# Performance work log

Hardware: AMD Instinct MI355X
Metric: run time of the kernel (lower is better)

The kernel has to match this reference:

```python
import jax, jax.numpy as jnp
import numpy as np

EMBED_DIM = 1024
NUM_HEADS = 16
HEAD_DIM = EMBED_DIM // NUM_HEADS  # 64
KV_RANK = 64
QK_RANK = 64
EPS = 1e-6


def rmsnorm(x, w):
    var = jnp.mean(x * x, axis=-1, keepdims=True)
    return x * jax.lax.rsqrt(var + EPS) * w


def setup_inputs() -> dict:
    key = jax.random.key(0)
    ks = jax.random.split(key, 6)
    B, N, C = 4, 2048, EMBED_DIM
    s = lambda fan_in: 1.0 / np.sqrt(fan_in)
    return {
        "x": jax.random.normal(ks[0], (B, N, C), dtype=jnp.float32),
        # nn.Linear weights stored as [out_features, in_features]
        "w_kv_a": jax.random.normal(ks[1], (KV_RANK, C), dtype=jnp.float32) * s(C),
        "w_kv_b": jax.random.normal(ks[2], (NUM_HEADS * HEAD_DIM * 2, KV_RANK), dtype=jnp.float32) * s(KV_RANK),
        "w_q_a": jax.random.normal(ks[3], (QK_RANK, C), dtype=jnp.float32) * s(C),
        "w_q_b": jax.random.normal(ks[4], (NUM_HEADS * HEAD_DIM, QK_RANK), dtype=jnp.float32) * s(QK_RANK),
        "w_proj": jax.random.normal(ks[5], (C, NUM_HEADS * HEAD_DIM), dtype=jnp.float32) * s(NUM_HEADS * HEAD_DIM),
        "kv_norm_w": jnp.ones((KV_RANK,), dtype=jnp.float32),
        "q_norm_w": jnp.ones((QK_RANK,), dtype=jnp.float32),
    }


def reference(x, w_kv_a, w_kv_b, w_q_a, w_q_b, w_proj, kv_norm_w, q_norm_w):
    B, N, C = x.shape
    H, D = NUM_HEADS, HEAD_DIM
    scale = D ** -0.5

    # low-rank KV path
    kv_latent = rmsnorm(x @ w_kv_a.T, kv_norm_w)              # [B,N,r]
    kv = (kv_latent @ w_kv_b.T).reshape(B, N, H, 2, D)
    k = kv[:, :, :, 0, :].transpose(0, 2, 1, 3)               # [B,H,N,D]
    v = kv[:, :, :, 1, :].transpose(0, 2, 1, 3)               # [B,H,N,D]

    # low-rank Q path
    q_latent = rmsnorm(x @ w_q_a.T, q_norm_w)                 # [B,N,r]
    q = (q_latent @ w_q_b.T).reshape(B, N, H, D).transpose(0, 2, 1, 3)

    attn = jnp.einsum("bhqd,bhkd->bhqk", q, k) * scale        # [B,H,N,N]
    attn = jax.nn.softmax(attn, axis=-1)
    y = jnp.einsum("bhqk,bhkd->bhqd", attn, v)                # [B,H,N,D]

    y = y.transpose(0, 2, 1, 3).reshape(B, N, H * D)
    return y @ w_proj.T
```

## Files before the change

### kernel.cpp

```cpp
#include <hip/hip_runtime.h>
#include <stdint.h>

typedef __bf16 bf16;
typedef __bf16 bf16x8 __attribute__((ext_vector_type(8)));
typedef __bf16 bf16x4 __attribute__((ext_vector_type(4)));
typedef float  f32x4  __attribute__((ext_vector_type(4)));

#define MFMA16(a,b,c) __builtin_amdgcn_mfma_f32_16x16x32_bf16((a),(b),(c),0,0,0)

__device__ __forceinline__ void gl16(const bf16* g, bf16* l) {
  __builtin_amdgcn_global_load_lds((const __attribute__((address_space(1))) void*)g,
                                   (__attribute__((address_space(3))) void*)l, 16, 0, 0);
}

#define OFF_XB     0LL
#define OFF_WAB    8388608LL
#define OFF_WKVB   8519680LL
#define OFF_WQB    8650752LL
#define OFF_WPROJ  8716288LL
#define OFF_LATN   9764864LL
#define OFF_K      10813440LL
#define OFF_VT     19202048LL
#define OFF_Q      27590656LL
#define OFF_Y      35979264LL

__global__ __launch_bounds__(256) void k_convert(
    const float* __restrict__ x, const float* __restrict__ wkva, const float* __restrict__ wkvb,
    const float* __restrict__ wqa, const float* __restrict__ wqb, const float* __restrict__ wproj,
    bf16* __restrict__ ws)
{
  int64_t q = (int64_t)blockIdx.x * 256 + threadIdx.x;
  const float* src; bf16* dst;
  if (q < 2097152LL)      { src = x + 4*q;                          dst = ws + OFF_XB + 4*q; }
  else if (q < 2129920LL) { int64_t e = 4*(q - 2097152LL);
                            int row = (int)(e >> 10), col = (int)(e & 1023);
                            src = (row < 64) ? (wkva + ((int64_t)row << 10) + col)
                                             : (wqa + ((int64_t)(row - 64) << 10) + col);
                            dst = ws + OFF_WAB + e; }
  else if (q < 2162688LL) { int64_t j = q - 2129920LL; src = wkvb + 4*j; dst = ws + OFF_WKVB + 4*j; }
  else if (q < 2179072LL) { int64_t j = q - 2162688LL; src = wqb  + 4*j; dst = ws + OFF_WQB  + 4*j; }
  else if (q < 2441216LL) { int64_t j = q - 2179072LL; src = wproj+ 4*j; dst = ws + OFF_WPROJ+ 4*j; }
  else return;
  float4 v = *(const float4*)src;
  bf16x4 o; o.x = (bf16)v.x; o.y = (bf16)v.y; o.z = (bf16)v.z; o.w = (bf16)v.w;
  *(bf16x4*)dst = o;
}

__device__ __forceinline__ void gemm_core(
    const bf16* __restrict__ A, const bf16* __restrict__ B,
    int lda, int ldb, int K, int m0, int n0,
    bf16* As, bf16* Bs, f32x4 acc[4][4])
{
  const int tid = threadIdx.x, lane = tid & 63;
  const int wr = tid >> 7, wc = (tid >> 6) & 1;
  const int r0 = tid >> 3, c0 = (tid & 7) * 8;
  const int csw = (((tid & 7) ^ (r0 & 7)) * 8);
  const int fr = lane & 15, fg = lane >> 4;
#pragma unroll
  for (int mi = 0; mi < 4; mi++)
#pragma unroll
    for (int ni = 0; ni < 4; ni++) acc[mi][ni] = (f32x4){0.f, 0.f, 0.f, 0.f};
  for (int kt = 0; kt < K; kt += 64) {
#pragma unroll
    for (int p = 0; p < 4; p++) {
      int row = p * 32 + r0;
      gl16(A + (int64_t)(m0 + row) * lda + kt + csw, As + row * 64 + c0);
      gl16(B + (int64_t)(n0 + row) * ldb + kt + csw, Bs + row * 64 + c0);
    }
    __syncthreads();
#pragma unroll
    for (int kk = 0; kk < 2; kk++) {
      bf16x8 af[4], bfr[4];
#pragma unroll
      for (int i = 0; i < 4; i++) {
        af[i]  = *(const bf16x8*)(As + (wr * 64 + i * 16 + fr) * 64 + (((kk * 4 + fg) ^ (fr & 7)) * 8));
        bfr[i] = *(const bf16x8*)(Bs + (wc * 64 + i * 16 + fr) * 64 + (((kk * 4 + fg) ^ (fr & 7)) * 8));
      }
#pragma unroll
      for (int mi = 0; mi < 4; mi++)
#pragma unroll
        for (int ni = 0; ni < 4; ni++)
          acc[mi][ni] = MFMA16(af[mi], bfr[ni], acc[mi][ni]);
    }
    __syncthreads();
  }
}

__global__ __launch_bounds__(256, 2) void k_latent(
    const bf16* __restrict__ xb, const bf16* __restrict__ wab,
    const float* __restrict__ kvw, const float* __restrict__ qw,
    bf16* __restrict__ latn)
{
  __shared__ bf16 As[128 * 64], Bs[128 * 64];
  f32x4 acc[4][4];
  const int m0 = blockIdx.x * 128;
  gemm_core(xb, wab, 1024, 1024, 1024, m0, 0, As, Bs, acc);
  const int tid = threadIdx.x, lane = tid & 63, wr = tid >> 7, wc = (tid >> 6) & 1;
  const int fr = lane & 15, fg = lane >> 4;
  const float* nw = wc ? qw : kvw;
  float wv[4];
#pragma unroll
  for (int ni = 0; ni < 4; ni++) wv[ni] = nw[ni * 16 + fr];
#pragma unroll
  for (int mi = 0; mi < 4; mi++) {
    f32x4 ss;
#pragma unroll
    for (int r = 0; r < 4; r++) {
      float s = 0.f;
#pragma unroll
      for (int ni = 0; ni < 4; ni++) { float v = acc[mi][ni][r]; s += v * v; }
      ss[r] = s;
    }
#pragma unroll
    for (int mask = 1; mask < 16; mask <<= 1)
#pragma unroll
      for (int r = 0; r < 4; r++) ss[r] += __shfl_xor(ss[r], mask, 64);
    f32x4 sc;
#pragma unroll
    for (int r = 0; r < 4; r++) sc[r] = rsqrtf(ss[r] * (1.f / 64.f) + 1e-6f);
#pragma unroll
    for (int ni = 0; ni < 4; ni++)
#pragma unroll
      for (int r = 0; r < 4; r++) {
        int row = m0 + wr * 64 + mi * 16 + fg * 4 + r;
        latn[(int64_t)row * 128 + wc * 64 + ni * 16 + fr] = (bf16)(acc[mi][ni][r] * sc[r] * wv[ni]);
      }
  }
}

__global__ __launch_bounds__(256, 2) void k_kv(
    const bf16* __restrict__ latn, const bf16* __restrict__ wkvb,
    bf16* __restrict__ kb, bf16* __restrict__ vtb)
{
  __shared__ bf16 As[128 * 64], Bs[128 * 64];
  f32x4 acc[4][4];
  const int m0 = blockIdx.x * 128, h = blockIdx.y;
  gemm_core(latn, wkvb, 128, 64, 64, m0, h * 128, As, Bs, acc);
  const int tid = threadIdx.x, lane = tid & 63, wr = tid >> 7, wc = (tid >> 6) & 1;
  const int fr = lane & 15, fg = lane >> 4;
#pragma unroll
  for (int mi = 0; mi < 4; mi++)
#pragma unroll
    for (int ni = 0; ni < 4; ni++)
#pragma unroll
      for (int r = 0; r < 4; r++) {
        int m = m0 + wr * 64 + mi * 16 + fg * 4 + r;
        int b = m >> 11, t = m & 2047;
        int c = ni * 16 + fr;
        bf16 v = (bf16)acc[mi][ni][r];
        if (wc == 0) kb [(int64_t)((b * 16 + h) * 2048 + t) * 64 + c] = v;
        else         vtb[(int64_t)((b * 16 + h) * 64 + c) * 2048 + t] = v;
      }
}

__global__ __launch_bounds__(256, 2) void k_q(
    const bf16* __restrict__ latn, const bf16* __restrict__ wqb,
    bf16* __restrict__ qbuf)
{
  __shared__ bf16 As[128 * 64], Bs[128 * 64];
  f32x4 acc[4][4];
  const int m0 = blockIdx.x * 128, n0 = blockIdx.y * 128;
  gemm_core(latn + 64, wqb, 128, 64, 64, m0, n0, As, Bs, acc);
  const int tid = threadIdx.x, lane = tid & 63, wr = tid >> 7, wc = (tid >> 6) & 1;
  const int fr = lane & 15, fg = lane >> 4;
#pragma unroll
  for (int mi = 0; mi < 4; mi++)
#pragma unroll
    for (int ni = 0; ni < 4; ni++)
#pragma unroll
      for (int r = 0; r < 4; r++) {
        int m = m0 + wr * 64 + mi * 16 + fg * 4 + r;
        int b = m >> 11, t = m & 2047;
        int n = n0 + wc * 64 + ni * 16 + fr;
        int hh = n >> 6, d = n & 63;
        qbuf[(int64_t)((b * 16 + hh) * 2048 + t) * 64 + d] = (bf16)(acc[mi][ni][r] * 0.125f);
      }
}

__global__ __launch_bounds__(256, 2) void k_attn(
    const bf16* __restrict__ qb, const bf16* __restrict__ kb,
    const bf16* __restrict__ vtb, bf16* __restrict__ yb)
{
  __shared__ bf16 Vts[64 * 128];
  __shared__ bf16 KsP[128 * 128];
  const int bh = blockIdx.x, qt = blockIdx.y;
  const int b = bh >> 4, h = bh & 15;
  const int tid = threadIdx.x, lane = tid & 63, w = tid >> 6;
  const int fr = lane & 15, fg = lane >> 4;
  const int64_t base = (int64_t)bh * (2048 * 64);
  bf16* Ks = KsP;
  bf16* Pw = KsP + w * 32 * 128;
  const int q0 = qt * 128 + w * 32;

  bf16x8 aq[2][2];
#pragma unroll
  for (int mi = 0; mi < 2; mi++)
#pragma unroll
    for (int kk = 0; kk < 2; kk++)
      aq[mi][kk] = *(const bf16x8*)(qb + base + (int64_t)(q0 + mi * 16 + fr) * 64 + kk * 32 + fg * 8);

  f32x4 o[2][4], mAcc[2], lAcc[2];
#pragma unroll
  for (int mi = 0; mi < 2; mi++) {
#pragma unroll
    for (int di = 0; di < 4; di++) o[mi][di] = (f32x4){0.f, 0.f, 0.f, 0.f};
#pragma unroll
    for (int r = 0; r < 4; r++) { mAcc[mi][r] = -__builtin_inff(); lAcc[mi][r] = 0.f; }
  }
  const int r0 = tid >> 3, c0 = (tid & 7) * 8;
  const int cswK = (((tid & 7) ^ (r0 & 7)) * 8);
  const int pcV = tid & 15, drB = (tid >> 4) & 7;
  const int cswV = ((pcV ^ drB) * 8);

  for (int kt = 0; kt < 16; kt++) {
    const int t0 = kt * 128;
#pragma unroll
    for (int p = 0; p < 4; p++) {
      int row = p * 32 + r0;
      gl16(kb + base + (int64_t)(t0 + row) * 64 + cswK, Ks + row * 64 + c0);
    }
#pragma unroll
    for (int p = 0; p < 4; p++) {
      int chunk = p * 256 + tid;
      int dr = chunk >> 4;
      gl16(vtb + base + (int64_t)dr * 2048 + t0 + cswV, Vts + dr * 128 + pcV * 8);
    }
    __syncthreads();
    f32x4 s[2][8];
#pragma unroll
    for (int mi = 0; mi < 2; mi++)
#pragma unroll
      for (int ni = 0; ni < 8; ni++) s[mi][ni] = (f32x4){0.f, 0.f, 0.f, 0.f};
#pragma unroll
    for (int kk = 0; kk < 2; kk++) {
      bf16x8 bk[8];
#pragma unroll
      for (int ni = 0; ni < 8; ni++)
        bk[ni] = *(const bf16x8*)(Ks + (ni * 16 + fr) * 64 + (((kk * 4 + fg) ^ (fr & 7)) * 8));
#pragma unroll
      for (int mi = 0; mi < 2; mi++)
#pragma unroll
        for (int ni = 0; ni < 8; ni++)
          s[mi][ni] = MFMA16(aq[mi][kk], bk[ni], s[mi][ni]);
    }
    __syncthreads();
#pragma unroll
    for (int mi = 0; mi < 2; mi++) {
      f32x4 pm;
#pragma unroll
      for (int r = 0; r < 4; r++) {
        float v = s[mi][0][r];
#pragma unroll
        for (int ni = 1; ni < 8; ni++) v = fmaxf(v, s[mi][ni][r]);
        pm[r] = v;
      }
#pragma unroll
      for (int mask = 1; mask < 16; mask <<= 1)
#pragma unroll
        for (int r = 0; r < 4; r++) pm[r] = fmaxf(pm[r], __shfl_xor(pm[r], mask, 64));
      f32x4 alpha, rs;
#pragma unroll
      for (int r = 0; r < 4; r++) {
        float mn = fmaxf(mAcc[mi][r], pm[r]);
        alpha[r] = exp2f((mAcc[mi][r] - mn) * 1.44269504f);
        mAcc[mi][r] = mn; rs[r] = 0.f;
      }
#pragma unroll
      for (int ni = 0; ni < 8; ni++)
#pragma unroll
        for (int r = 0; r < 4; r++) {
          float p = exp2f((s[mi][ni][r] - mAcc[mi][r]) * 1.44269504f);
          rs[r] += p;
          int rp = mi * 16 + fg * 4 + r;
          int c  = ni * 16 + fr;
          Pw[rp * 128 + ((((c >> 3) ^ (rp & 7)) << 3) | (c & 7))] = (bf16)p;
        }
#pragma unroll
      for (int mask = 1; mask < 16; mask <<= 1)
#pragma unroll
        for (int r = 0; r < 4; r++) rs[r] += __shfl_xor(rs[r], mask, 64);
#pragma unroll
      for (int r = 0; r < 4; r++) lAcc[mi][r] = lAcc[mi][r] * alpha[r] + rs[r];
#pragma unroll
      for (int di = 0; di < 4; di++)
#pragma unroll
        for (int r = 0; r < 4; r++) o[mi][di][r] *= alpha[r];
    }
#pragma unroll
    for (int k2 = 0; k2 < 4; k2++) {
      bf16x8 pa[2], vv[4];
#pragma unroll
      for (int mi = 0; mi < 2; mi++)
        pa[mi] = *(const bf16x8*)(Pw + (mi * 16 + fr) * 128 + (((k2 * 4 + fg) ^ (fr & 7)) * 8));
#pragma unroll
      for (int di = 0; di < 4; di++)
        vv[di] = *(const bf16x8*)(Vts + (di * 16 + fr) * 128 + (((k2 * 4 + fg) ^ (fr & 7)) * 8));
#pragma unroll
      for (int mi = 0; mi < 2; mi++)
#pragma unroll
        for (int di = 0; di < 4; di++)
          o[mi][di] = MFMA16(pa[mi], vv[di], o[mi][di]);
    }
    __syncthreads();
  }
#pragma unroll
  for (int mi = 0; mi < 2; mi++)
#pragma unroll
    for (int di = 0; di < 4; di++)
#pragma unroll
      for (int r = 0; r < 4; r++) {
        int t = q0 + mi * 16 + fg * 4 + r;
        float v = o[mi][di][r] / lAcc[mi][r];
        yb[((int64_t)b * 2048 + t) * 1024 + h * 64 + di * 16 + fr] = (bf16)v;
      }
}

__global__ __launch_bounds__(256, 2) void k_proj(
    const bf16* __restrict__ yb, const bf16* __restrict__ wp, float* __restrict__ out)
{
  __shared__ bf16 As[128 * 64], Bs[128 * 64];
  f32x4 acc[4][4];
  const int m0 = blockIdx.x * 128, n0 = blockIdx.y * 128;
  gemm_core(yb, wp, 1024, 1024, 1024, m0, n0, As, Bs, acc);
  const int tid = threadIdx.x, lane = tid & 63, wr = tid >> 7, wc = (tid >> 6) & 1;
  const int fr = lane & 15, fg = lane >> 4;
#pragma unroll
  for (int mi = 0; mi < 4; mi++)
#pragma unroll
    for (int ni = 0; ni < 4; ni++)
#pragma unroll
      for (int r = 0; r < 4; r++) {
        int m = m0 + wr * 64 + mi * 16 + fg * 4 + r;
        int n = n0 + wc * 64 + ni * 16 + fr;
        out[(int64_t)m * 1024 + n] = acc[mi][ni][r];
      }
}

extern "C" void kernel_launch(void* const* d_in, const int* in_sizes, int n_in,
                              void* d_out, int out_size, void* d_ws, size_t ws_size,
                              hipStream_t stream) {
  (void)in_sizes; (void)n_in; (void)out_size; (void)ws_size;
  const float* x     = (const float*)d_in[0];
  const float* wkva  = (const float*)d_in[1];
  const float* wkvb  = (const float*)d_in[2];
  const float* wqa   = (const float*)d_in[3];
  const float* wqb   = (const float*)d_in[4];
  const float* wproj = (const float*)d_in[5];
  const float* kvw   = (const float*)d_in[6];
  const float* qw    = (const float*)d_in[7];
  bf16* ws  = (bf16*)d_ws;
  float* out = (float*)d_out;

  k_convert<<<dim3(9536), dim3(256), 0, stream>>>(x, wkva, wkvb, wqa, wqb, wproj, ws);
  k_latent <<<dim3(64), dim3(256), 0, stream>>>(ws + OFF_XB, ws + OFF_WAB, kvw, qw, ws + OFF_LATN);
  k_kv     <<<dim3(64, 16), dim3(256), 0, stream>>>(ws + OFF_LATN, ws + OFF_WKVB, ws + OFF_K, ws + OFF_VT);
  k_q      <<<dim3(64, 8), dim3(256), 0, stream>>>(ws + OFF_LATN, ws + OFF_WQB, ws + OFF_Q);
  k_attn   <<<dim3(64, 16), dim3(256), 0, stream>>>(ws + OFF_Q, ws + OFF_K, ws + OFF_VT, ws + OFF_Y);
  k_proj   <<<dim3(64, 8), dim3(256), 0, stream>>>(ws + OFF_Y, ws + OFF_WPROJ, out);
}
```

Baseline: 358.0 us.

## Compute transposed QK^T so softmax rows live per lane, packing P stores

```diff
diff --git a/kernel.cpp b/kernel.cpp
--- a/kernel.cpp
+++ b/kernel.cpp
@@ -7,6 +7,7 @@
 typedef float  f32x4  __attribute__((ext_vector_type(4)));
 
 #define MFMA16(a,b,c) __builtin_amdgcn_mfma_f32_16x16x32_bf16((a),(b),(c),0,0,0)
+#define LOG2E 1.44269504f
 
 __device__ __forceinline__ void gl16(const bf16* g, bf16* l) {
   __builtin_amdgcn_global_load_lds((const __attribute__((address_space(1))) void*)g,
@@ -187,6 +188,7 @@
   const int b = bh >> 4, h = bh & 15;
   const int tid = threadIdx.x, lane = tid & 63, w = tid >> 6;
   const int fr = lane & 15, fg = lane >> 4;
+  const int fg4 = fg * 4;
   const int64_t base = (int64_t)bh * (2048 * 64);
   bf16* Ks = KsP;
   bf16* Pw = KsP + w * 32 * 128;
@@ -199,13 +201,13 @@
     for (int kk = 0; kk < 2; kk++)
       aq[mi][kk] = *(const bf16x8*)(qb + base + (int64_t)(q0 + mi * 16 + fr) * 64 + kk * 32 + fg * 8);
 
-  f32x4 o[2][4], mAcc[2], lAcc[2];
+  f32x4 o[2][4];
+  float mS[2], lS[2];
 #pragma unroll
   for (int mi = 0; mi < 2; mi++) {
 #pragma unroll
     for (int di = 0; di < 4; di++) o[mi][di] = (f32x4){0.f, 0.f, 0.f, 0.f};
-#pragma unroll
-    for (int r = 0; r < 4; r++) { mAcc[mi][r] = -__builtin_inff(); lAcc[mi][r] = 0.f; }
+    mS[mi] = -__builtin_inff(); lS[mi] = 0.f;
   }
   const int r0 = tid >> 3, c0 = (tid & 7) * 8;
   const int cswK = (((tid & 7) ^ (r0 & 7)) * 8);
@@ -226,11 +228,11 @@
       gl16(vtb + base + (int64_t)dr * 2048 + t0 + cswV, Vts + dr * 128 + pcV * 8);
     }
     __syncthreads();
-    f32x4 s[2][8];
+    f32x4 sT[2][8];
 #pragma unroll
     for (int mi = 0; mi < 2; mi++)
 #pragma unroll
-      for (int ni = 0; ni < 8; ni++) s[mi][ni] = (f32x4){0.f, 0.f, 0.f, 0.f};
+      for (int ni = 0; ni < 8; ni++) sT[mi][ni] = (f32x4){0.f, 0.f, 0.f, 0.f};
 #pragma unroll
     for (int kk = 0; kk < 2; kk++) {
       bf16x8 bk[8];
@@ -241,51 +243,48 @@
       for (int mi = 0; mi < 2; mi++)
 #pragma unroll
         for (int ni = 0; ni < 8; ni++)
-          s[mi][ni] = MFMA16(aq[mi][kk], bk[ni], s[mi][ni]);
+          sT[mi][ni] = MFMA16(bk[ni], aq[mi][kk], sT[mi][ni]);
     }
     __syncthreads();
 #pragma unroll
     for (int mi = 0; mi < 2; mi++) {
-      f32x4 pm;
-#pragma unroll
-      for (int r = 0; r < 4; r++) {
-        float v = s[mi][0][r];
-#pragma unroll
-        for (int ni = 1; ni < 8; ni++) v = fmaxf(v, s[mi][ni][r]);
-        pm[r] = v;
-      }
-#pragma unroll
-      for (int mask = 1; mask < 16; mask <<= 1)
-#pragma unroll
-        for (int r = 0; r < 4; r++) pm[r] = fmaxf(pm[r], __shfl_xor(pm[r], mask, 64));
-      f32x4 alpha, rs;
-#pragma unroll
-      for (int r = 0; r < 4; r++) {
-        float mn = fmaxf(mAcc[mi][r], pm[r]);
-        alpha[r] = exp2f((mAcc[mi][r] - mn) * 1.44269504f);
-        mAcc[mi][r] = mn; rs[r] = 0.f;
-      }
+      float pm = sT[mi][0][0];
 #pragma unroll
       for (int ni = 0; ni < 8; ni++)
 #pragma unroll
-        for (int r = 0; r < 4; r++) {
-          float p = exp2f((s[mi][ni][r] - mAcc[mi][r]) * 1.44269504f);
-          rs[r] += p;
-          int rp = mi * 16 + fg * 4 + r;
-          int c  = ni * 16 + fr;
-          Pw[rp * 128 + ((((c >> 3) ^ (rp & 7)) << 3) | (c & 7))] = (bf16)p;
-        }
-#pragma unroll
-      for (int mask = 1; mask < 16; mask <<= 1)
-#pragma unroll
-        for (int r = 0; r < 4; r++) rs[r] += __shfl_xor(rs[r], mask, 64);
-#pragma unroll
-      for (int r = 0; r < 4; r++) lAcc[mi][r] = lAcc[mi][r] * alpha[r] + rs[r];
+        for (int r = 0; r < 4; r++) pm = fmaxf(pm, sT[mi][ni][r]);
+      pm = fmaxf(pm, __shfl_xor(pm, 16, 64));
+      pm = fmaxf(pm, __shfl_xor(pm, 32, 64));
+      float mn = fmaxf(mS[mi], pm);
+      float alphaS = exp2f((mS[mi] - mn) * LOG2E);
+      mS[mi] = mn;
+      const float mnL = mn * LOG2E;
+      float rs = 0.f;
+      bf16* pwr = Pw + (mi * 16 + fr) * 128 + (fg & 1) * 4;
+      const int cxor = fr & 7;
+#pragma unroll
+      for (int ni = 0; ni < 8; ni++) {
+        float p0 = exp2f(fmaf(sT[mi][ni][0], LOG2E, -mnL));
+        float p1 = exp2f(fmaf(sT[mi][ni][1], LOG2E, -mnL));
+        float p2 = exp2f(fmaf(sT[mi][ni][2], LOG2E, -mnL));
+        float p3 = exp2f(fmaf(sT[mi][ni][3], LOG2E, -mnL));
+        rs += (p0 + p1) + (p2 + p3);
+        bf16x4 pk4;
+        pk4[0] = (bf16)p0; pk4[1] = (bf16)p1; pk4[2] = (bf16)p2; pk4[3] = (bf16)p3;
+        *(bf16x4*)(pwr + (((ni * 2 + (fg >> 1)) ^ cxor) << 3)) = pk4;
+      }
+      rs += __shfl_xor(rs, 16, 64);
+      rs += __shfl_xor(rs, 32, 64);
+      lS[mi] = lS[mi] * alphaS + rs;
+      float aO[4];
+#pragma unroll
+      for (int r = 0; r < 4; r++) aO[r] = __shfl(alphaS, fg4 + r, 64);
 #pragma unroll
       for (int di = 0; di < 4; di++)
 #pragma unroll
-        for (int r = 0; r < 4; r++) o[mi][di][r] *= alpha[r];
-    }
+        for (int r = 0; r < 4; r++) o[mi][di][r] *= aO[r];
+    }
+    __syncthreads();
 #pragma unroll
     for (int k2 = 0; k2 < 4; k2++) {
       bf16x8 pa[2], vv[4];
@@ -304,15 +303,19 @@
     __syncthreads();
   }
 #pragma unroll
-  for (int mi = 0; mi < 2; mi++)
+  for (int mi = 0; mi < 2; mi++) {
+    float lO[4];
+#pragma unroll
+    for (int r = 0; r < 4; r++) lO[r] = __shfl(lS[mi], fg4 + r, 64);
 #pragma unroll
     for (int di = 0; di < 4; di++)
 #pragma unroll
       for (int r = 0; r < 4; r++) {
         int t = q0 + mi * 16 + fg * 4 + r;
-        float v = o[mi][di][r] / lAcc[mi][r];
+        float v = o[mi][di][r] / lO[r];
         yb[((int64_t)b * 2048 + t) * 1024 + h * 64 + di * 16 + fr] = (bf16)v;
       }
+  }
 }
 
 __global__ __launch_bounds__(256, 2) void k_proj(
```

New measurement: 304.6 us. -14.9%, faster.
